# Optimization experiments

Hardware: AMD Instinct MI355X
Metric: run time of the kernel (lower is better)

## Reference

```python
import jax, jax.numpy as jnp
import numpy as np

B, S, D, H = 2, 2048, 1024, 16
HD = D // H  # head_features = 64
MASKED_BIAS = -10000.0


def setup_inputs() -> dict:
    key = jax.random.key(0)
    ks = jax.random.split(key, 5)
    return {
        "hidden_states": jax.random.normal(ks[0], (B, S, D), dtype=jnp.float32),
        "c_attn_w": jax.random.normal(ks[1], (D, 3 * D), dtype=jnp.float32) * 0.02,
        "c_attn_b": jax.random.normal(ks[2], (3 * D,), dtype=jnp.float32) * 0.02,
        "c_proj_w": jax.random.normal(ks[3], (D, D), dtype=jnp.float32) * 0.02,
        "c_proj_b": jax.random.normal(ks[4], (D,), dtype=jnp.float32) * 0.02,
    }


def reference(hidden_states, c_attn_w, c_attn_b, c_proj_w, c_proj_b):
    b, s, d = hidden_states.shape
    # Conv1D: x @ W + b, projecting D -> 3D, then split into q, k, v
    qkv = hidden_states @ c_attn_w + c_attn_b  # [b, s, 3D]
    q, k, v = jnp.split(qkv, 3, axis=-1)
    # split heads -> [b, H, s, HD]
    q = q.reshape(b, s, H, HD).transpose(0, 2, 1, 3)
    k = k.reshape(b, s, H, HD).transpose(0, 2, 1, 3)
    v = v.reshape(b, s, H, HD).transpose(0, 2, 1, 3)
    # scaled scores: [b, H, s, s]
    w = jnp.einsum("bhqd,bhkd->bhqk", q, k) / jnp.sqrt(jnp.float32(HD))
    # causal mask (tril bias buffer) applied via where with masked_bias
    causal = jnp.tril(jnp.ones((s, s), dtype=bool))
    w = jnp.where(causal[None, None], w, jnp.float32(MASKED_BIAS))
    p = jax.nn.softmax(w, axis=-1)  # attn_dropout p=0
    a = jnp.einsum("bhqk,bhkd->bhqd", p, v)  # [b, H, s, HD]
    # merge heads -> [b, s, D], output projection (resid_dropout p=0)
    a = a.transpose(0, 2, 1, 3).reshape(b, s, d)
    return a @ c_proj_w + c_proj_b
```

## Files before the change

kernel.cpp:

```cpp
#include <hip/hip_runtime.h>

typedef unsigned short u16;
typedef unsigned int   u32;

typedef __attribute__((ext_vector_type(8))) short bf16x8;
typedef __attribute__((ext_vector_type(4))) short bf16x4;
typedef __attribute__((ext_vector_type(4))) float f32x4;

typedef const __attribute__((address_space(1))) u32 gq_t;
typedef __attribute__((address_space(3))) u32 lq_t;

__device__ __forceinline__ float b2f(u16 u) {
    union { u32 u; float f; } c; c.u = ((u32)u) << 16; return c.f;
}
__device__ __forceinline__ u16 f2b(float f) {
    union { float f; u32 u; } c; c.f = f;
    u32 r = c.u + 0x7fffu + ((c.u >> 16) & 1u);
    return (u16)(r >> 16);
}
__device__ __forceinline__ u16 f2b_hu(float f) {
    union { float f; u32 u; } c; c.f = f;
    return (u16)((c.u + 0x8000u) >> 16);
}

__global__ __launch_bounds__(256) void prep(
    const float* __restrict__ X,    u16* __restrict__ Xb,
    const float* __restrict__ Wqkv, u16* __restrict__ WqkvT,
    const float* __restrict__ Wp,   u16* __restrict__ WprojT)
{
    __shared__ float t[32][33];
    const int bid = blockIdx.x, tid = threadIdx.x;
    if (bid < 2048) {
        const int i = (bid * 256 + tid) * 8;
        f32x4 a = *(const f32x4*)(X + i);
        f32x4 b = *(const f32x4*)(X + i + 4);
        union { bf16x8 v; u16 u[8]; } o;
        o.u[0] = f2b(a[0]); o.u[1] = f2b(a[1]); o.u[2] = f2b(a[2]); o.u[3] = f2b(a[3]);
        o.u[4] = f2b(b[0]); o.u[5] = f2b(b[1]); o.u[6] = f2b(b[2]); o.u[7] = f2b(b[3]);
        *(bf16x8*)(Xb + i) = o.v;
        return;
    }
    const float* in; u16* out; int N, bx, by;
    if (bid < 5120) { const int b2 = bid - 2048; in = Wqkv; out = WqkvT; N = 3072; bx = b2 % 96; by = b2 / 96; }
    else            { const int b3 = bid - 5120; in = Wp;   out = WprojT; N = 1024; bx = b3 & 31; by = b3 >> 5; }
    const int k0 = by * 32, n0 = bx * 32;
    const int kr = tid >> 3, nc = (tid & 7) * 4;
    f32x4 v = *(const f32x4*)(in + (size_t)(k0 + kr) * N + n0 + nc);
    t[kr][nc] = v[0]; t[kr][nc + 1] = v[1]; t[kr][nc + 2] = v[2]; t[kr][nc + 3] = v[3];
    __syncthreads();
    const int nr = tid >> 3, kc = (tid & 7) * 4;
    union { bf16x4 v; u16 a[4]; } o;
    o.a[0] = f2b(t[kc][nr]);     o.a[1] = f2b(t[kc + 1][nr]);
    o.a[2] = f2b(t[kc + 2][nr]); o.a[3] = f2b(t[kc + 3][nr]);
    *(bf16x4*)(out + (size_t)(n0 + nr) * 1024 + k0 + kc) = o.v;
}


__global__ __launch_bounds__(256) void gemm128(
    const u16* __restrict__ A, const u16* __restrict__ WT,
    const float* __restrict__ bias, float* __restrict__ out,
    u16* __restrict__ Qb, u16* __restrict__ Kb, u16* __restrict__ Vt,
    int N, int K, int mode)
{
    __shared__ u16 As[128 * 32];
    __shared__ u16 Bs[128 * 32];
    const int tid  = threadIdx.x;
    const int m0   = blockIdx.y * 128, n0 = blockIdx.x * 128;
    const int wv   = tid >> 6, lane = tid & 63;
    const int wm   = (wv >> 1) * 64, wn = (wv & 1) * 64;
    const int l16  = lane & 15, quad = lane >> 4;

    const int sr = lane >> 2;
    const int sc = (((lane & 3) ^ ((lane >> 3) & 3)) * 8);
    const int rbase = wv * 16 + sr;
    const int rsw = ((l16 >> 1) & 3) * 8;

    f32x4 acc[4][4];
    const f32x4 zero = {0.f, 0.f, 0.f, 0.f};
    #pragma unroll
    for (int i = 0; i < 4; i++)
        #pragma unroll
        for (int j = 0; j < 4; j++) acc[i][j] = zero;

    for (int k0 = 0; k0 < K; k0 += 32) {
        #pragma unroll
        for (int c = 0; c < 2; c++) {
            const int rl = c * 64 + rbase;
            const u16* ag = A  + (size_t)(m0 + rl) * K + k0 + sc;
            const u16* bg = WT + (size_t)(n0 + rl) * K + k0 + sc;
            __builtin_amdgcn_global_load_lds((gq_t*)ag, (lq_t*)&As[(c * 64 + wv * 16) * 32], 16, 0, 0);
            __builtin_amdgcn_global_load_lds((gq_t*)bg, (lq_t*)&Bs[(c * 64 + wv * 16) * 32], 16, 0, 0);
        }
        __syncthreads();
        bf16x8 af[4], bf[4];
        #pragma unroll
        for (int i = 0; i < 4; i++) {
            af[i] = *(const bf16x8*)&As[(wm + i * 16 + l16) * 32 + ((quad * 8) ^ rsw)];
            bf[i] = *(const bf16x8*)&Bs[(wn + i * 16 + l16) * 32 + ((quad * 8) ^ rsw)];
        }
        #pragma unroll
        for (int i = 0; i < 4; i++)
            #pragma unroll
            for (int j = 0; j < 4; j++)
                acc[i][j] = __builtin_amdgcn_mfma_f32_16x16x32_bf16(af[i], bf[j], acc[i][j], 0, 0, 0);
        __syncthreads();
    }

    #pragma unroll
    for (int j = 0; j < 4; j++) {
        const int nn = n0 + wn + j * 16 + l16;
        const float bvf = bias[nn];
        #pragma unroll
        for (int i = 0; i < 4; i++) {
            float o[4];
            #pragma unroll
            for (int r = 0; r < 4; r++) o[r] = acc[i][j][r] + bvf;
            const int mbase = m0 + wm + i * 16 + quad * 4;
            if (mode == 0) {
                #pragma unroll
                for (int r = 0; r < 4; r++)
                    out[(size_t)(mbase + r) * N + nn] = o[r];
            } else {
                const int part = nn >> 10, w = nn & 1023;
                const int h = w >> 6, d = w & 63;
                const int b = mbase >> 11, s = mbase & 2047;
                const size_t bh = (size_t)b * 16 + h;
                if (part == 2) {
                    union { bf16x4 v; u16 a[4]; } pk;
                    #pragma unroll
                    for (int r = 0; r < 4; r++) pk.a[r] = f2b(o[r]);
                    *(bf16x4*)(Vt + (bh * 64 + d) * 2048 + s) = pk.v;
                } else {
                    u16* t = (part == 0) ? Qb : Kb;
                    const float scl = (part == 0) ? 0.125f : 1.0f;
                    #pragma unroll
                    for (int r = 0; r < 4; r++)
                        t[(bh * 2048 + s + r) * 64 + d] = f2b(o[r] * scl);
                }
            }
        }
    }
}

__global__ __launch_bounds__(256) void gemm_proj(
    const u16* __restrict__ A, const u16* __restrict__ WT,
    const float* __restrict__ bias, float* __restrict__ out, int N, int K)
{
    __shared__ u16 As[128 * 32];
    __shared__ u16 Bs[64 * 32];
    const int tid  = threadIdx.x;
    const int m0   = blockIdx.y * 128, n0 = blockIdx.x * 64;
    const int wv   = tid >> 6, lane = tid & 63;
    const int wm   = (wv >> 1) * 64, wn = (wv & 1) * 32;
    const int l16  = lane & 15, quad = lane >> 4;

    const int sr = lane >> 2;
    const int sc = (((lane & 3) ^ ((lane >> 3) & 3)) * 8);
    const int rbase = wv * 16 + sr;
    const int rsw = ((l16 >> 1) & 3) * 8;

    f32x4 acc[4][2];
    const f32x4 zero = {0.f, 0.f, 0.f, 0.f};
    #pragma unroll
    for (int i = 0; i < 4; i++) { acc[i][0] = zero; acc[i][1] = zero; }

    for (int k0 = 0; k0 < K; k0 += 32) {
        #pragma unroll
        for (int c = 0; c < 2; c++) {
            const u16* ag = A + (size_t)(m0 + c * 64 + rbase) * K + k0 + sc;
            __builtin_amdgcn_global_load_lds((gq_t*)ag, (lq_t*)&As[(c * 64 + wv * 16) * 32], 16, 0, 0);
        }
        const u16* bg = WT + (size_t)(n0 + rbase) * K + k0 + sc;
        __builtin_amdgcn_global_load_lds((gq_t*)bg, (lq_t*)&Bs[(wv * 16) * 32], 16, 0, 0);
        __syncthreads();
        bf16x8 af[4], bf[2];
        #pragma unroll
        for (int i = 0; i < 4; i++)
            af[i] = *(const bf16x8*)&As[(wm + i * 16 + l16) * 32 + ((quad * 8) ^ rsw)];
        #pragma unroll
        for (int j = 0; j < 2; j++)
            bf[j] = *(const bf16x8*)&Bs[(wn + j * 16 + l16) * 32 + ((quad * 8) ^ rsw)];
        #pragma unroll
        for (int i = 0; i < 4; i++)
            #pragma unroll
            for (int j = 0; j < 2; j++)
                acc[i][j] = __builtin_amdgcn_mfma_f32_16x16x32_bf16(af[i], bf[j], acc[i][j], 0, 0, 0);
        __syncthreads();
    }

    #pragma unroll
    for (int j = 0; j < 2; j++) {
        const int nn = n0 + wn + j * 16 + l16;
        const float bvf = bias[nn];
        #pragma unroll
        for (int i = 0; i < 4; i++) {
            const int mbase = m0 + wm + i * 16 + quad * 4;
            #pragma unroll
            for (int r = 0; r < 4; r++)
                out[(size_t)(mbase + r) * N + nn] = acc[i][j][r] + bvf;
        }
    }
}

__global__ __launch_bounds__(256, 3) void attn_mfma(
    const u16* __restrict__ Qb, const u16* __restrict__ Kb,
    const u16* __restrict__ Vt, u16* __restrict__ Aout)
{
    const int bx   = blockIdx.x;
    const int x    = bx & 511, half = bx >> 9;
    const int xcd  = x & 7, y = x >> 3;
    const int bh   = xcd * 4 + (y & 3);
    const int pidx = y >> 2;
    const int chunk = half ? (31 - pidx) : pidx;
    const int q0   = chunk * 64;

    const int tid  = threadIdx.x;
    const int wave = tid >> 6, lane = tid & 63;
    const int l16  = lane & 15, quad = lane >> 4;
    const int qw   = q0 + wave * 16;
    const size_t kbase = (size_t)bh * 2048 * 64;
    const size_t vbase = (size_t)bh * 64 * 2048;

    __shared__ __align__(16) u16 Ks[2][64 * 72];
    __shared__ __align__(16) u16 Vs[2][64 * 72];
    __shared__ __align__(16) u16 p_all[4][16 * 72];
    u16* p_lds = p_all[wave];

    const u16* qp = Qb + kbase + (size_t)(qw + l16) * 64 + quad * 8;
    bf16x8 aq0 = *(const bf16x8*)qp;
    bf16x8 aq1 = *(const bf16x8*)(qp + 32);

    union { bf16x8 v; u16 a[8]; } onesu;
    #pragma unroll
    for (int j = 0; j < 8; j++) onesu.a[j] = 0x3F80;
    const bf16x8 vones = onesu.v;

    f32x4 oacc[4], lacc;
    const f32x4 zero = {0.f, 0.f, 0.f, 0.f};
    #pragma unroll
    for (int t = 0; t < 4; t++) oacc[t] = zero;
    lacc = zero;

    const int srow = tid >> 2, scol = (tid & 3) * 16;
    u16* ksw0 = &Ks[0][srow * 72 + scol];
    u16* vsw0 = &Vs[0][srow * 72 + scol];
    u16* ksw1 = &Ks[1][srow * 72 + scol];
    u16* vsw1 = &Vs[1][srow * 72 + scol];

    {
        const u16* kg = Kb + kbase + (size_t)srow * 64 + scol;
        const u16* vg = Vt + vbase + (size_t)srow * 2048 + scol;
        bf16x8 k0 = *(const bf16x8*)kg, k1 = *(const bf16x8*)(kg + 8);
        bf16x8 v0 = *(const bf16x8*)vg, v1 = *(const bf16x8*)(vg + 8);
        *(bf16x8*)ksw0 = k0; *(bf16x8*)(ksw0 + 8) = k1;
        *(bf16x8*)vsw0 = v0; *(bf16x8*)(vsw0 + 8) = v1;
    }
    __syncthreads();

    for (int kt = 0; kt <= chunk; kt++) {
        const int kb = kt * 64, buf = kt & 1;

        bf16x8 pk0, pk1, pv0, pv1;
        const bool pf = (kt < chunk);
        if (pf) {
            const u16* kg = Kb + kbase + (size_t)(kb + 64 + srow) * 64 + scol;
            const u16* vg = Vt + vbase + (size_t)srow * 2048 + (kb + 64) + scol;
            pk0 = *(const bf16x8*)kg; pk1 = *(const bf16x8*)(kg + 8);
            pv0 = *(const bf16x8*)vg; pv1 = *(const bf16x8*)(vg + 8);
        }

        const u16* Kl = Ks[buf];
        const u16* Vl = Vs[buf];
        bf16x8 kk[8], vv[8];
        #pragma unroll
        for (int t = 0; t < 4; t++) {
            #pragma unroll
            for (int ks = 0; ks < 2; ks++) {
                kk[2 * t + ks] = *(const bf16x8*)&Kl[(16 * t + l16) * 72 + ks * 32 + quad * 8];
                vv[2 * t + ks] = *(const bf16x8*)&Vl[(16 * t + l16) * 72 + ks * 32 + quad * 8];
            }
        }

        f32x4 sc[4];
        #pragma unroll
        for (int t = 0; t < 4; t++) {
            sc[t] = __builtin_amdgcn_mfma_f32_16x16x32_bf16(aq0, kk[2 * t],     zero,  0, 0, 0);
            sc[t] = __builtin_amdgcn_mfma_f32_16x16x32_bf16(aq1, kk[2 * t + 1], sc[t], 0, 0, 0);
        }

        const bool diag = (kt == chunk);
        #pragma unroll
        for (int r = 0; r < 4; r++) {
            const int qi = qw + quad * 4 + r;
            u16* pw = &p_lds[(quad * 4 + r) * 72 + l16];
            #pragma unroll
            for (int t = 0; t < 4; t++) {
                float pv = __expf(sc[t][r]);
                if (diag && (kb + 16 * t + l16 > qi)) pv = 0.f;
                pw[16 * t] = f2b_hu(pv);
            }
        }

        __asm__ volatile("s_waitcnt lgkmcnt(0)");

        #pragma unroll
        for (int ks = 0; ks < 2; ks++) {
            bf16x8 ap = *(const bf16x8*)&p_lds[l16 * 72 + ks * 32 + quad * 8];
            #pragma unroll
            for (int t = 0; t < 4; t++)
                oacc[t] = __builtin_amdgcn_mfma_f32_16x16x32_bf16(ap, vv[2 * t + ks], oacc[t], 0, 0, 0);
            lacc = __builtin_amdgcn_mfma_f32_16x16x32_bf16(ap, vones, lacc, 0, 0, 0);
        }

        if (pf) {
            if (buf) { *(bf16x8*)ksw0 = pk0; *(bf16x8*)(ksw0 + 8) = pk1;
                       *(bf16x8*)vsw0 = pv0; *(bf16x8*)(vsw0 + 8) = pv1; }
            else     { *(bf16x8*)ksw1 = pk0; *(bf16x8*)(ksw1 + 8) = pk1;
                       *(bf16x8*)vsw1 = pv0; *(bf16x8*)(vsw1 + 8) = pv1; }
        }
        __syncthreads();
    }

    const int b = bh >> 4, h = bh & 15;
    #pragma unroll
    for (int r = 0; r < 4; r++) {
        const float inv = 1.0f / lacc[r];
        const int qi = qw + quad * 4 + r;
        u16* dst = Aout + (size_t)(b * 2048 + qi) * 1024 + h * 64 + l16;
        #pragma unroll
        for (int t = 0; t < 4; t++)
            dst[16 * t] = f2b(oacc[t][r] * inv);
    }
}

extern "C" void kernel_launch(void* const* d_in, const int* in_sizes, int n_in,
                              void* d_out, int out_size, void* d_ws, size_t ws_size,
                              hipStream_t stream)
{
    const float* X    = (const float*)d_in[0];
    const float* Wqkv = (const float*)d_in[1];
    const float* Bqkv = (const float*)d_in[2];
    const float* Wp   = (const float*)d_in[3];
    const float* Bp   = (const float*)d_in[4];
    float* out = (float*)d_out;

    char* ws = (char*)d_ws;
    u16* WqkvT = (u16*)(ws);
    u16* WprojT= (u16*)(ws + 6291456);
    u16* Qb    = (u16*)(ws + 8388608);
    u16* Kb    = (u16*)(ws + 16777216);
    u16* Vt    = (u16*)(ws + 25165824);
    u16* Ab    = (u16*)(ws + 33554432);
    u16* Xb    = (u16*)(ws + 41943040);

    prep<<<dim3(6144), 256, 0, stream>>>(X, Xb, Wqkv, WqkvT, Wp, WprojT);

    gemm128<<<dim3(24, 32), 256, 0, stream>>>(Xb, WqkvT, Bqkv, nullptr,
                                              Qb, Kb, Vt, 3072, 1024, 1);
    attn_mfma<<<dim3(1024), 256, 0, stream>>>(Qb, Kb, Vt, Ab);
    gemm_proj<<<dim3(16, 32), 256, 0, stream>>>(Ab, WprojT, Bp, out, 1024, 1024);
}
```

Measured before the change: 178.4 us.

## Double QKV GEMM K-tile, single-buffer attention LDS, cheaper bf16 rounding

The QKV GEMM now stages a 64-wide K slice per iteration with a new XOR swizzle, which halves the number of barrier pairs and loop trips. The attention kernel drops its double-buffered K/V LDS for a single buffer, adding an extra barrier per tile, and raises the occupancy hint to 4 blocks per CU. Several bf16 conversions switch to the cheaper round-half-up form. The single buffer trades K/V load overlap for occupancy, and the rounding change slightly alters numerics.

```diff
diff --git a/kernel.cpp b/kernel.cpp
--- a/kernel.cpp
+++ b/kernel.cpp
@@ -55,25 +55,23 @@
     *(bf16x4*)(out + (size_t)(n0 + nr) * 1024 + k0 + kc) = o.v;
 }
 
-
 __global__ __launch_bounds__(256) void gemm128(
     const u16* __restrict__ A, const u16* __restrict__ WT,
     const float* __restrict__ bias, float* __restrict__ out,
     u16* __restrict__ Qb, u16* __restrict__ Kb, u16* __restrict__ Vt,
     int N, int K, int mode)
 {
-    __shared__ u16 As[128 * 32];
-    __shared__ u16 Bs[128 * 32];
+    __shared__ u16 As[128 * 64];
+    __shared__ u16 Bs[128 * 64];
     const int tid  = threadIdx.x;
     const int m0   = blockIdx.y * 128, n0 = blockIdx.x * 128;
     const int wv   = tid >> 6, lane = tid & 63;
     const int wm   = (wv >> 1) * 64, wn = (wv & 1) * 64;
     const int l16  = lane & 15, quad = lane >> 4;
 
-    const int sr = lane >> 2;
-    const int sc = (((lane & 3) ^ ((lane >> 3) & 3)) * 8);
-    const int rbase = wv * 16 + sr;
-    const int rsw = ((l16 >> 1) & 3) * 8;
+    const int srow = tid >> 3;
+    const int slog = ((tid & 7) ^ (srow & 7)) * 8;
+    const int rsw8 = l16 & 7;
 
     f32x4 acc[4][4];
     const f32x4 zero = {0.f, 0.f, 0.f, 0.f};
@@ -82,27 +80,30 @@
         #pragma unroll
         for (int j = 0; j < 4; j++) acc[i][j] = zero;
 
-    for (int k0 = 0; k0 < K; k0 += 32) {
-        #pragma unroll
-        for (int c = 0; c < 2; c++) {
-            const int rl = c * 64 + rbase;
-            const u16* ag = A  + (size_t)(m0 + rl) * K + k0 + sc;
-            const u16* bg = WT + (size_t)(n0 + rl) * K + k0 + sc;
-            __builtin_amdgcn_global_load_lds((gq_t*)ag, (lq_t*)&As[(c * 64 + wv * 16) * 32], 16, 0, 0);
-            __builtin_amdgcn_global_load_lds((gq_t*)bg, (lq_t*)&Bs[(c * 64 + wv * 16) * 32], 16, 0, 0);
-        }
-        __syncthreads();
-        bf16x8 af[4], bf[4];
-        #pragma unroll
-        for (int i = 0; i < 4; i++) {
-            af[i] = *(const bf16x8*)&As[(wm + i * 16 + l16) * 32 + ((quad * 8) ^ rsw)];
-            bf[i] = *(const bf16x8*)&Bs[(wn + i * 16 + l16) * 32 + ((quad * 8) ^ rsw)];
-        }
-        #pragma unroll
-        for (int i = 0; i < 4; i++)
-            #pragma unroll
-            for (int j = 0; j < 4; j++)
-                acc[i][j] = __builtin_amdgcn_mfma_f32_16x16x32_bf16(af[i], bf[j], acc[i][j], 0, 0, 0);
+    for (int k0 = 0; k0 < K; k0 += 64) {
+        #pragma unroll
+        for (int c = 0; c < 4; c++) {
+            const u16* ag = A  + (size_t)(m0 + c * 32 + srow) * K + k0 + slog;
+            const u16* bg = WT + (size_t)(n0 + c * 32 + srow) * K + k0 + slog;
+            __builtin_amdgcn_global_load_lds((gq_t*)ag, (lq_t*)&As[c * 2048 + wv * 512], 16, 0, 0);
+            __builtin_amdgcn_global_load_lds((gq_t*)bg, (lq_t*)&Bs[c * 2048 + wv * 512], 16, 0, 0);
+        }
+        __syncthreads();
+        #pragma unroll
+        for (int ks = 0; ks < 2; ks++) {
+            const int ph = (((ks * 4 + quad) ^ rsw8) * 8);
+            bf16x8 af[4], bfr[4];
+            #pragma unroll
+            for (int i = 0; i < 4; i++) {
+                af[i]  = *(const bf16x8*)&As[(wm + i * 16 + l16) * 64 + ph];
+                bfr[i] = *(const bf16x8*)&Bs[(wn + i * 16 + l16) * 64 + ph];
+            }
+            #pragma unroll
+            for (int i = 0; i < 4; i++)
+                #pragma unroll
+                for (int j = 0; j < 4; j++)
+                    acc[i][j] = __builtin_amdgcn_mfma_f32_16x16x32_bf16(af[i], bfr[j], acc[i][j], 0, 0, 0);
+        }
         __syncthreads();
     }
 
@@ -128,14 +129,14 @@
                 if (part == 2) {
                     union { bf16x4 v; u16 a[4]; } pk;
                     #pragma unroll
-                    for (int r = 0; r < 4; r++) pk.a[r] = f2b(o[r]);
+                    for (int r = 0; r < 4; r++) pk.a[r] = f2b_hu(o[r]);
                     *(bf16x4*)(Vt + (bh * 64 + d) * 2048 + s) = pk.v;
                 } else {
                     u16* t = (part == 0) ? Qb : Kb;
                     const float scl = (part == 0) ? 0.125f : 1.0f;
                     #pragma unroll
                     for (int r = 0; r < 4; r++)
-                        t[(bh * 2048 + s + r) * 64 + d] = f2b(o[r] * scl);
+                        t[(bh * 2048 + s + r) * 64 + d] = f2b_hu(o[r] * scl);
                 }
             }
         }
@@ -173,18 +174,18 @@
         const u16* bg = WT + (size_t)(n0 + rbase) * K + k0 + sc;
         __builtin_amdgcn_global_load_lds((gq_t*)bg, (lq_t*)&Bs[(wv * 16) * 32], 16, 0, 0);
         __syncthreads();
-        bf16x8 af[4], bf[2];
+        bf16x8 af[4], bfr[2];
         #pragma unroll
         for (int i = 0; i < 4; i++)
             af[i] = *(const bf16x8*)&As[(wm + i * 16 + l16) * 32 + ((quad * 8) ^ rsw)];
         #pragma unroll
         for (int j = 0; j < 2; j++)
-            bf[j] = *(const bf16x8*)&Bs[(wn + j * 16 + l16) * 32 + ((quad * 8) ^ rsw)];
+            bfr[j] = *(const bf16x8*)&Bs[(wn + j * 16 + l16) * 32 + ((quad * 8) ^ rsw)];
         #pragma unroll
         for (int i = 0; i < 4; i++)
             #pragma unroll
             for (int j = 0; j < 2; j++)
-                acc[i][j] = __builtin_amdgcn_mfma_f32_16x16x32_bf16(af[i], bf[j], acc[i][j], 0, 0, 0);
+                acc[i][j] = __builtin_amdgcn_mfma_f32_16x16x32_bf16(af[i], bfr[j], acc[i][j], 0, 0, 0);
         __syncthreads();
     }
 
@@ -202,7 +203,7 @@
     }
 }
 
-__global__ __launch_bounds__(256, 3) void attn_mfma(
+__global__ __launch_bounds__(256, 4) void attn_mfma(
     const u16* __restrict__ Qb, const u16* __restrict__ Kb,
     const u16* __restrict__ Vt, u16* __restrict__ Aout)
 {
@@ -221,8 +222,8 @@
     const size_t kbase = (size_t)bh * 2048 * 64;
     const size_t vbase = (size_t)bh * 64 * 2048;
 
-    __shared__ __align__(16) u16 Ks[2][64 * 72];
-    __shared__ __align__(16) u16 Vs[2][64 * 72];
+    __shared__ __align__(16) u16 Ks[64 * 72];
+    __shared__ __align__(16) u16 Vs[64 * 72];
     __shared__ __align__(16) u16 p_all[4][16 * 72];
     u16* p_lds = p_all[wave];
 
@@ -242,26 +243,24 @@
     lacc = zero;
 
     const int srow = tid >> 2, scol = (tid & 3) * 16;
-    u16* ksw0 = &Ks[0][srow * 72 + scol];
-    u16* vsw0 = &Vs[0][srow * 72 + scol];
-    u16* ksw1 = &Ks[1][srow * 72 + scol];
-    u16* vsw1 = &Vs[1][srow * 72 + scol];
+    u16* ksw = &Ks[srow * 72 + scol];
+    u16* vsw = &Vs[srow * 72 + scol];
 
     {
         const u16* kg = Kb + kbase + (size_t)srow * 64 + scol;
         const u16* vg = Vt + vbase + (size_t)srow * 2048 + scol;
         bf16x8 k0 = *(const bf16x8*)kg, k1 = *(const bf16x8*)(kg + 8);
         bf16x8 v0 = *(const bf16x8*)vg, v1 = *(const bf16x8*)(vg + 8);
-        *(bf16x8*)ksw0 = k0; *(bf16x8*)(ksw0 + 8) = k1;
-        *(bf16x8*)vsw0 = v0; *(bf16x8*)(vsw0 + 8) = v1;
+        *(bf16x8*)ksw = k0; *(bf16x8*)(ksw + 8) = k1;
+        *(bf16x8*)vsw = v0; *(bf16x8*)(vsw + 8) = v1;
     }
     __syncthreads();
 
     for (int kt = 0; kt <= chunk; kt++) {
-        const int kb = kt * 64, buf = kt & 1;
+        const int kb = kt * 64;
+        const bool pf = (kt < chunk);
 
         bf16x8 pk0, pk1, pv0, pv1;
-        const bool pf = (kt < chunk);
         if (pf) {
             const u16* kg = Kb + kbase + (size_t)(kb + 64 + srow) * 64 + scol;
             const u16* vg = Vt + vbase + (size_t)srow * 2048 + (kb + 64) + scol;
@@ -269,15 +268,13 @@
             pv0 = *(const bf16x8*)vg; pv1 = *(const bf16x8*)(vg + 8);
         }
 
-        const u16* Kl = Ks[buf];
-        const u16* Vl = Vs[buf];
         bf16x8 kk[8], vv[8];
         #pragma unroll
         for (int t = 0; t < 4; t++) {
             #pragma unroll
             for (int ks = 0; ks < 2; ks++) {
-                kk[2 * t + ks] = *(const bf16x8*)&Kl[(16 * t + l16) * 72 + ks * 32 + quad * 8];
-                vv[2 * t + ks] = *(const bf16x8*)&Vl[(16 * t + l16) * 72 + ks * 32 + quad * 8];
+                kk[2 * t + ks] = *(const bf16x8*)&Ks[(16 * t + l16) * 72 + ks * 32 + quad * 8];
+                vv[2 * t + ks] = *(const bf16x8*)&Vs[(16 * t + l16) * 72 + ks * 32 + quad * 8];
             }
         }
 
@@ -312,13 +309,12 @@
             lacc = __builtin_amdgcn_mfma_f32_16x16x32_bf16(ap, vones, lacc, 0, 0, 0);
         }
 
+        __syncthreads();
         if (pf) {
-            if (buf) { *(bf16x8*)ksw0 = pk0; *(bf16x8*)(ksw0 + 8) = pk1;
-                       *(bf16x8*)vsw0 = pv0; *(bf16x8*)(vsw0 + 8) = pv1; }
-            else     { *(bf16x8*)ksw1 = pk0; *(bf16x8*)(ksw1 + 8) = pk1;
-                       *(bf16x8*)vsw1 = pv0; *(bf16x8*)(vsw1 + 8) = pv1; }
-        }
-        __syncthreads();
+            *(bf16x8*)ksw = pk0; *(bf16x8*)(ksw + 8) = pk1;
+            *(bf16x8*)vsw = pv0; *(bf16x8*)(vsw + 8) = pv1;
+            __syncthreads();
+        }
     }
 
     const int b = bh >> 4, h = bh & 15;
@@ -329,7 +325,7 @@
         u16* dst = Aout + (size_t)(b * 2048 + qi) * 1024 + h * 64 + l16;
         #pragma unroll
         for (int t = 0; t < 4; t++)
-            dst[16 * t] = f2b(oacc[t][r] * inv);
+            dst[16 * t] = f2b_hu(oacc[t][r] * inv);
     }
 }
 
```

After: 172.9 us. 3.1% less time.
